# Kernel tuning notes

Measured on AMD Instinct MI355X. Metric: run time of the kernel, lower is better.

Reference implementation:

```python
import jax, jax.numpy as jnp
import numpy as np

VTH = 1.0      # v_threshold
TAU = 2.0      # spikingjelly LIFNode default tau
ALPHA = 2.0    # ATan surrogate alpha
EPS = 1e-5     # BatchNorm eps
N_HEADS = 8
TOPK = 4       # routed regions per query region
REGION = 64    # tokens per region (4096 tokens -> 64 regions)


@jax.custom_vjp
def spike_fn(v):
    return (v >= VTH).astype(v.dtype)

def _spike_fwd(v):
    return (v >= VTH).astype(v.dtype), v

def _spike_bwd(v, g):
    sg = (ALPHA / 2.0) / (1.0 + (jnp.pi / 2.0 * ALPHA * (v - VTH)) ** 2)
    return (g * sg,)

spike_fn.defvjp(_spike_fwd, _spike_bwd)


def lif(x):
    # x: [T, B, L, D]; LIF with decay_input=True, hard reset to 0, detach_reset
    def step(v, xt):
        v = v + (xt - v) / TAU
        s = spike_fn(v)
        v = v * (1.0 - jax.lax.stop_gradient(s))
        return v, s
    _, s = jax.lax.scan(step, jnp.zeros_like(x[0]), x)
    return s


def batchnorm(x, gamma, beta):
    # torch BN1d over [T*B, D, L] in training mode == per-channel stats over (T,B,L)
    mean = x.mean(axis=(0, 1, 2))
    var = jnp.mean((x - mean) ** 2, axis=(0, 1, 2))
    return (x - mean) * jax.lax.rsqrt(var + EPS) * gamma + beta


def bilevel_attn(x, qkv_w, qkv_b, proj_w, proj_b):
    # x: [TB, L, D]
    TB, L, D = x.shape
    nreg = L // REGION
    hd = D // N_HEADS
    qkv = x @ qkv_w.T + qkv_b
    q, k, v = jnp.split(qkv, 3, axis=-1)
    qr = q.reshape(TB, nreg, REGION, D)
    kr = k.reshape(TB, nreg, REGION, D)
    vr = v.reshape(TB, nreg, REGION, D)
    # coarse region-level routing via mean-pooled q/k affinity
    aff = jnp.einsum('bnd,bmd->bnm', qr.mean(2), kr.mean(2))  # [TB, nreg, nreg]
    _, idx = jax.lax.top_k(aff, TOPK)                         # [TB, nreg, TOPK]
    gather = jax.vmap(lambda t, ix: t[ix])                    # per-sample region gather
    kg = gather(kr, idx).reshape(TB, nreg, TOPK * REGION, N_HEADS, hd)
    vg = gather(vr, idx).reshape(TB, nreg, TOPK * REGION, N_HEADS, hd)
    qh = qr.reshape(TB, nreg, REGION, N_HEADS, hd)
    logits = jnp.einsum('bnqhd,bnkhd->bnhqk', qh, kg) * (hd ** -0.5)
    p = jax.nn.softmax(logits, axis=-1)
    o = jnp.einsum('bnhqk,bnkhd->bnqhd', p, vg).reshape(TB, L, D)
    return o @ proj_w.T + proj_b


def setup_inputs() -> dict:
    key = jax.random.key(0)
    ks = jax.random.split(key, 8)
    T, B, Lt, L, D = 4, 2, 4, 1024, 256
    Ltot = Lt * L
    s = 0.02
    return {
        'x': jax.random.normal(ks[0], (T, B, Ltot, D), jnp.float32),
        'bn1_g': jnp.ones((D,), jnp.float32),
        'bn1_b': jnp.zeros((D,), jnp.float32),
        'bn2_g': jnp.ones((D,), jnp.float32),
        'bn2_b': jnp.zeros((D,), jnp.float32),
        'qkv_w': jax.random.normal(ks[1], (3 * D, D), jnp.float32) * s,
        'qkv_b': jnp.zeros((3 * D,), jnp.float32),
        'proj_w': jax.random.normal(ks[2], (D, D), jnp.float32) * s,
        'proj_b': jnp.zeros((D,), jnp.float32),
        'ffn_w1': jax.random.normal(ks[3], (4 * D, D), jnp.float32) * s,
        'ffn_b1': jnp.zeros((4 * D,), jnp.float32),
        'ffn_w2': jax.random.normal(ks[4], (D, 4 * D), jnp.float32) * s,
        'ffn_b2': jnp.zeros((D,), jnp.float32),
        'scale': jnp.ones((1,), jnp.float32) * 0.5,
        'Lt': Lt, 'b': B, 'L': L, 'dim': D,
    }


def reference(x, bn1_g, bn1_b, bn2_g, bn2_b, qkv_w, qkv_b, proj_w, proj_b,
              ffn_w1, ffn_b1, ffn_w2, ffn_b2, scale, Lt, b, L, dim):
    T = x.shape[0]
    Ltot = Lt * L
    # attention branch
    identity = x
    s1 = lif(batchnorm(x, bn1_g, bn1_b))
    a = bilevel_attn(s1.reshape(T * b, Ltot, dim), qkv_w, qkv_b, proj_w, proj_b)
    x = identity + a.reshape(T, b, Ltot, dim) * scale
    # ffn branch
    s2 = lif(batchnorm(x, bn2_g, bn2_b))
    h = jax.nn.gelu(s2 @ ffn_w1.T + ffn_b1, approximate=False) @ ffn_w2.T + ffn_b2
    return x + h * scale
```

## Files before the change

kernel.cpp:

```cpp
#include <hip/hip_runtime.h>
#include <hip/hip_bf16.h>
#include <math.h>

typedef __attribute__((ext_vector_type(8))) short short8;
typedef __attribute__((ext_vector_type(4))) float f32x4;

#define DIM 256
#define NROWS 32768
#define PERT 2097152
#define SAMP_TOK 4096

__device__ __forceinline__ float b2f(__hip_bfloat16 h){ return __bfloat162float(h); }
__device__ __forceinline__ __hip_bfloat16 f2b(float f){ return __float2bfloat16(f); }
__device__ __forceinline__ unsigned short f2bu(float f){
  __hip_bfloat16 h = __float2bfloat16(f);
  unsigned short u; __builtin_memcpy(&u, &h, 2); return u;
}

#define GLD_LDS16(gp, lp) __builtin_amdgcn_global_load_lds( \
    (const __attribute__((address_space(1))) unsigned int*)(gp), \
    (__attribute__((address_space(3))) unsigned int*)(lp), 16, 0, 0)

__device__ __forceinline__ float gelu_fast(float v){
  float z  = v * 0.70710678118654752f;
  float az = fabsf(z);
  float t  = __builtin_amdgcn_rcpf(fmaf(0.3275911f, az, 1.0f));
  float p  = fmaf(fmaf(fmaf(fmaf(1.061405429f, t, -1.453152027f), t,
                            1.421413741f), t, -0.284496736f), t, 0.254829592f);
  p *= t;
  float e  = __expf(-z * z);
  float y  = fmaf(-p, e, 1.0f);
  return fmaf(0.5f * fabsf(v), y, 0.5f * v);
}

__global__ void f2b_k(const float* __restrict__ in, __hip_bfloat16* __restrict__ out, int n){
  int i = blockIdx.x * 256 + threadIdx.x;
  if (i < n) out[i] = f2b(in[i]);
}

__global__ void bn_stats_k(const float* __restrict__ x, float* __restrict__ sum, float* __restrict__ sumsq){
  int c = threadIdx.x;
  size_t base = (size_t)blockIdx.x * 64 * DIM + c;
  float s = 0.f, s2 = 0.f;
  for (int i = 0; i < 64; ++i){
    float v = x[base + (size_t)i * DIM];
    s += v; s2 += v * v;
  }
  atomicAdd(&sum[c], s);
  atomicAdd(&sumsq[c], s2);
}

__global__ void bn_fin_k(const float* __restrict__ sum, const float* __restrict__ sumsq,
                         const float* __restrict__ g, const float* __restrict__ b,
                         float* __restrict__ a_out, float* __restrict__ b_out){
  int c = threadIdx.x;
  float mean = sum[c] * (1.f/32768.f);
  float var  = sumsq[c] * (1.f/32768.f) - mean*mean;
  float a = g[c] / sqrtf(var + 1e-5f);
  a_out[c] = a;
  b_out[c] = b[c] - mean * a;
}

__global__ void lif_k(const float* __restrict__ x, const float* __restrict__ av,
                      const float* __restrict__ bv, __hip_bfloat16* __restrict__ s){
  int e = blockIdx.x * blockDim.x + threadIdx.x;
  if (e >= PERT) return;
  int c = e & (DIM - 1);
  float a = av[c], b = bv[c];
  float v = 0.f;
  #pragma unroll
  for (int t = 0; t < 4; ++t){
    float xn = x[(size_t)t * PERT + e] * a + b;
    v += (xn - v) * 0.5f;
    float sp = (v >= 1.0f) ? 1.0f : 0.0f;
    s[(size_t)t * PERT + e] = f2b(sp);
    v = (v >= 1.0f) ? 0.f : v;
  }
}

__global__ void region_sum_k(const __hip_bfloat16* __restrict__ s, float* __restrict__ sm){
  int r = blockIdx.x, c = threadIdx.x;
  float acc = 0.f;
  size_t base = (size_t)r * 64 * DIM + c;
  for (int i = 0; i < 64; ++i) acc += b2f(s[base + (size_t)i * DIM]);
  sm[(size_t)r * DIM + c] = acc * 0.015625f;
}

__global__ void rgemm_k(const float* __restrict__ smr, const float* __restrict__ w,
                        const float* __restrict__ bias, float* __restrict__ qkm){
  __shared__ float arow[256];
  int r = blockIdx.x, t = threadIdx.x;
  arow[t] = smr[(size_t)r * 256 + t];
  __syncthreads();
  for (int j = t; j < 512; j += 256){
    const float* wr = w + (size_t)j * 256;
    float acc = 0.f;
    for (int k = 0; k < 256; ++k) acc += arow[k] * wr[k];
    qkm[(size_t)r * 512 + j] = acc + bias[j];
  }
}

template<int EPI>
__global__ __launch_bounds__(256) void gemm_bt(
    const __hip_bfloat16* __restrict__ A, const __hip_bfloat16* __restrict__ W,
    const float* __restrict__ bias, void* __restrict__ outp,
    const void* __restrict__ extra, const float* __restrict__ scaleptr,
    int K, int N)
{
  __shared__ __align__(16) short As[128 * 32];
  __shared__ __align__(16) short Ws[128 * 32];
  int tid = threadIdx.x;
  int bm = blockIdx.x, bn = blockIdx.y;
  int lane = tid & 63;
  int l16 = lane & 15, quad = lane >> 4;
  int wv = tid >> 6;
  int wm = (wv >> 1) << 6, wn = (wv & 1) << 6;

  const __hip_bfloat16* Ag = A + (size_t)(bm * 128 + (tid >> 2)) * K + ((tid & 3) << 3);
  const __hip_bfloat16* Wg = W + (size_t)(bn * 128 + (tid >> 2)) * K + ((tid & 3) << 3);
  short* Ad = As + tid * 8;
  short* Wd = Ws + tid * 8;
  const size_t rstep = (size_t)64 * K;

  f32x4 zero = {0.f, 0.f, 0.f, 0.f};
  f32x4 acc[4][4];
  #pragma unroll
  for (int i = 0; i < 4; ++i)
    #pragma unroll
    for (int j = 0; j < 4; ++j) acc[i][j] = zero;

  for (int k0 = 0; k0 < K; k0 += 32){
    GLD_LDS16(Ag + k0,         Ad);
    GLD_LDS16(Ag + rstep + k0, Ad + 2048);
    GLD_LDS16(Wg + k0,         Wd);
    GLD_LDS16(Wg + rstep + k0, Wd + 2048);
    __syncthreads();
    short8 af[4];
    #pragma unroll
    for (int mi = 0; mi < 4; ++mi)
      af[mi] = *reinterpret_cast<const short8*>(&As[(wm + mi * 16 + l16) * 32 + (quad << 3)]);
    #pragma unroll
    for (int ni = 0; ni < 4; ++ni){
      short8 wf = *reinterpret_cast<const short8*>(&Ws[(wn + ni * 16 + l16) * 32 + (quad << 3)]);
      #pragma unroll
      for (int mi = 0; mi < 4; ++mi)
        acc[mi][ni] = __builtin_amdgcn_mfma_f32_16x16x32_bf16(wf, af[mi], acc[mi][ni], 0, 0, 0);
    }
    __syncthreads();
  }

  float sc = 0.f;
  if (EPI == 1 || EPI == 3) sc = scaleptr[0];
  #pragma unroll
  for (int ni = 0; ni < 4; ++ni){
    int col0 = (bn << 7) + wn + ni * 16 + (quad << 2);
    float4 bv = *reinterpret_cast<const float4*>(bias + col0);
    #pragma unroll
    for (int mi = 0; mi < 4; ++mi){
      int rowg = (bm << 7) + wm + mi * 16 + l16;
      size_t off = (size_t)rowg * N + col0;
      float v0 = acc[mi][ni][0] + bv.x;
      float v1 = acc[mi][ni][1] + bv.y;
      float v2 = acc[mi][ni][2] + bv.z;
      float v3 = acc[mi][ni][3] + bv.w;
      if (EPI == 0){
        unsigned lo = (unsigned)f2bu(v0) | ((unsigned)f2bu(v1) << 16);
        unsigned hi = (unsigned)f2bu(v2) | ((unsigned)f2bu(v3) << 16);
        *reinterpret_cast<uint2*>((__hip_bfloat16*)outp + off) = make_uint2(lo, hi);
      } else if (EPI == 1 || EPI == 3){
        float4 xr = *reinterpret_cast<const float4*>((const float*)extra + off);
        float4 ov;
        ov.x = xr.x + v0 * sc; ov.y = xr.y + v1 * sc;
        ov.z = xr.z + v2 * sc; ov.w = xr.w + v3 * sc;
        *reinterpret_cast<float4*>((float*)outp + off) = ov;
      } else {
        float g0 = gelu_fast(v0), g1 = gelu_fast(v1);
        float g2 = gelu_fast(v2), g3 = gelu_fast(v3);
        unsigned lo = (unsigned)f2bu(g0) | ((unsigned)f2bu(g1) << 16);
        unsigned hi = (unsigned)f2bu(g2) | ((unsigned)f2bu(g3) << 16);
        *reinterpret_cast<uint2*>((__hip_bfloat16*)outp + off) = make_uint2(lo, hi);
      }
    }
  }
}

__global__ void topk_k(const float* __restrict__ qkm, int* __restrict__ idx){
  __shared__ float aff[64];
  int r = blockIdx.x;
  int m = threadIdx.x;
  int b = r >> 6;
  const float4* qrow = reinterpret_cast<const float4*>(qkm + (size_t)r * 512);
  const float4* krow = reinterpret_cast<const float4*>(qkm + (size_t)(b * 64 + m) * 512 + 256);
  float dot = 0.f;
  for (int d = 0; d < 64; ++d){
    float4 qv = qrow[d], kv = krow[d];
    dot += qv.x * kv.x + qv.y * kv.y + qv.z * kv.z + qv.w * kv.w;
  }
  aff[m] = dot;
  __syncthreads();
  if (m == 0){
    #pragma unroll
    for (int t = 0; t < 4; ++t){
      float best = -INFINITY; int bi = 0;
      for (int i = 0; i < 64; ++i){
        if (aff[i] > best){ best = aff[i]; bi = i; }
      }
      aff[bi] = -INFINITY;
      idx[r * 4 + t] = bi;
    }
  }
}

__global__ __launch_bounds__(256) void attn_mfma_k(
    const __hip_bfloat16* __restrict__ qkv, const int* __restrict__ idx,
    __hip_bfloat16* __restrict__ o_out, int rbase)
{
  __shared__ __align__(16) short lds[27136];
  __shared__ float den_s[4][16];
  const int rl = blockIdx.x;
  const int h  = blockIdx.y;
  const int rg = rbase + rl;
  const int bl = rl >> 6;
  const int tid = threadIdx.x;
  const int w = tid >> 6, lane = tid & 63;
  const int l16 = lane & 15, quad = lane >> 4;
  short* Pw = lds + 10240 + w * 4224;

  const int reg = idx[rg * 4 + (tid >> 6)] & 63;
  const size_t srow = (size_t)bl * SAMP_TOK + (size_t)reg * 64 + (tid & 63);
  const __hip_bfloat16* kvsrc = qkv + srow * 768 + 256 + (size_t)h * 32;

  const size_t qrow = (size_t)rl * 64 + w * 16 + l16;
  short8 qf = *reinterpret_cast<const short8*>(qkv + qrow * 768 + (size_t)h * 32 + quad * 8);

  uint4 vreg[4];
  #pragma unroll
  for (int c = 0; c < 4; ++c)
    vreg[c] = *reinterpret_cast<const uint4*>(kvsrc + 256 + c * 8);

  #pragma unroll
  for (int c = 0; c < 4; ++c)
    *reinterpret_cast<uint4*>(&lds[tid * 40 + c * 8]) =
      *reinterpret_cast<const uint4*>(kvsrc + c * 8);
  __syncthreads();

  f32x4 s[16];
  #pragma unroll
  for (int nt = 0; nt < 16; ++nt){
    short8 bf = *reinterpret_cast<const short8*>(&lds[(nt * 16 + l16) * 40 + quad * 8]);
    f32x4 z = {0.f, 0.f, 0.f, 0.f};
    s[nt] = __builtin_amdgcn_mfma_f32_16x16x32_bf16(qf, bf, z, 0, 0, 0);
  }
  __syncthreads();

  #pragma unroll
  for (int c = 0; c < 4; ++c){
    short8 vv = *reinterpret_cast<short8*>(&vreg[c]);
    #pragma unroll
    for (int e = 0; e < 8; ++e)
      lds[(c * 8 + e) * 264 + tid] = vv[e];
  }

  float m4[4] = {-1e30f, -1e30f, -1e30f, -1e30f};
  #pragma unroll
  for (int nt = 0; nt < 16; ++nt)
    #pragma unroll
    for (int r = 0; r < 4; ++r) m4[r] = fmaxf(m4[r], s[nt][r]);
  #pragma unroll
  for (int xm = 1; xm < 16; xm <<= 1)
    #pragma unroll
    for (int r = 0; r < 4; ++r) m4[r] = fmaxf(m4[r], __shfl_xor(m4[r], xm));
  float d4[4] = {0.f, 0.f, 0.f, 0.f};
  #pragma unroll
  for (int nt = 0; nt < 16; ++nt)
    #pragma unroll
    for (int r = 0; r < 4; ++r){
      float e = __expf((s[nt][r] - m4[r]) * 0.17677669529663687f);
      s[nt][r] = e; d4[r] += e;
    }
  #pragma unroll
  for (int xm = 1; xm < 16; xm <<= 1)
    #pragma unroll
    for (int r = 0; r < 4; ++r) d4[r] += __shfl_xor(d4[r], xm);
  if (l16 == 0){
    #pragma unroll
    for (int r = 0; r < 4; ++r) den_s[w][quad * 4 + r] = d4[r];
  }
  #pragma unroll
  for (int nt = 0; nt < 16; ++nt)
    #pragma unroll
    for (int r = 0; r < 4; ++r)
      Pw[(quad * 4 + r) * 264 + nt * 16 + l16] = (short)f2bu(s[nt][r]);
  __syncthreads();

  f32x4 o0 = {0.f, 0.f, 0.f, 0.f}, o1 = o0;
  #pragma unroll
  for (int kk = 0; kk < 8; ++kk){
    short8 pb = *reinterpret_cast<const short8*>(&Pw[l16 * 264 + kk * 32 + quad * 8]);
    short8 a0 = *reinterpret_cast<const short8*>(&lds[l16 * 264 + kk * 32 + quad * 8]);
    short8 a1 = *reinterpret_cast<const short8*>(&lds[(16 + l16) * 264 + kk * 32 + quad * 8]);
    o0 = __builtin_amdgcn_mfma_f32_16x16x32_bf16(a0, pb, o0, 0, 0, 0);
    o1 = __builtin_amdgcn_mfma_f32_16x16x32_bf16(a1, pb, o1, 0, 0, 0);
  }
  float inv = 1.f / den_s[w][l16];
  size_t obase = ((size_t)rl * 64 + w * 16 + l16) * 256 + (size_t)h * 32;
  unsigned pk0 = (unsigned)f2bu(o0[0] * inv) | ((unsigned)f2bu(o0[1] * inv) << 16);
  unsigned pk1 = (unsigned)f2bu(o0[2] * inv) | ((unsigned)f2bu(o0[3] * inv) << 16);
  unsigned pk2 = (unsigned)f2bu(o1[0] * inv) | ((unsigned)f2bu(o1[1] * inv) << 16);
  unsigned pk3 = (unsigned)f2bu(o1[2] * inv) | ((unsigned)f2bu(o1[3] * inv) << 16);
  *reinterpret_cast<uint2*>(o_out + obase + quad * 4)      = make_uint2(pk0, pk1);
  *reinterpret_cast<uint2*>(o_out + obase + 16 + quad * 4) = make_uint2(pk2, pk3);
}

extern "C" void kernel_launch(void* const* d_in, const int* in_sizes, int n_in,
                              void* d_out, int out_size, void* d_ws, size_t ws_size,
                              hipStream_t stream)
{
  const float* x      = (const float*)d_in[0];
  const float* bn1_g  = (const float*)d_in[1];
  const float* bn1_b  = (const float*)d_in[2];
  const float* bn2_g  = (const float*)d_in[3];
  const float* bn2_b  = (const float*)d_in[4];
  const float* qkv_w  = (const float*)d_in[5];
  const float* qkv_b  = (const float*)d_in[6];
  const float* proj_w = (const float*)d_in[7];
  const float* proj_b = (const float*)d_in[8];
  const float* ffn_w1 = (const float*)d_in[9];
  const float* ffn_b1 = (const float*)d_in[10];
  const float* ffn_w2 = (const float*)d_in[11];
  const float* ffn_b2 = (const float*)d_in[12];
  const float* scale  = (const float*)d_in[13];
  float* x2 = (float*)d_out;

  char* ws = (char*)d_ws;
  const size_t MB = 1024 * 1024;
  float* sum1 = (float*)(ws + 0);
  float* sq1  = (float*)(ws + 1024);
  float* sum2 = (float*)(ws + 2048);
  float* sq2  = (float*)(ws + 3072);
  float* a1   = (float*)(ws + 4096);
  float* b1   = (float*)(ws + 5120);
  float* a2   = (float*)(ws + 6144);
  float* b2   = (float*)(ws + 7168);
  int*   idxb = (int*)(ws + 8192);
  float* smr  = (float*)(ws + 16384);
  float* qkm  = (float*)(ws + 540672);
  __hip_bfloat16* qkv_wb  = (__hip_bfloat16*)(ws + 1589248);
  __hip_bfloat16* proj_wb = (__hip_bfloat16*)(ws + 1982464);
  __hip_bfloat16* ffn_w1b = (__hip_bfloat16*)(ws + 2113536);
  __hip_bfloat16* ffn_w2b = (__hip_bfloat16*)(ws + 2637824);
  __hip_bfloat16* s1 = (__hip_bfloat16*)(ws + 4 * MB);
  __hip_bfloat16* s2 = s1;
  char* chunkbuf = ws + 20 * MB;

  size_t avail = (ws_size > 20 * MB) ? (ws_size - 20 * MB) : (8 * MB);
  int nc = (avail >= 64 * MB) ? 8 : (avail >= 32 * MB) ? 4 : (avail >= 16 * MB) ? 2 : 1;
  int crows = 32768;
  while ((size_t)crows * 2048 > avail && crows > 2048) crows >>= 1;

  __hip_bfloat16* qkvc = (__hip_bfloat16*)chunkbuf;
  __hip_bfloat16* oc   = (__hip_bfloat16*)(chunkbuf + (size_t)nc * 6 * MB);
  __hip_bfloat16* h1   = (__hip_bfloat16*)chunkbuf;

  hipMemsetAsync(d_ws, 0, 4096, stream);

  f2b_k<<<(196608 + 255) / 256, 256, 0, stream>>>(qkv_w, qkv_wb, 196608);
  f2b_k<<<(65536 + 255) / 256, 256, 0, stream>>>(proj_w, proj_wb, 65536);
  f2b_k<<<(262144 + 255) / 256, 256, 0, stream>>>(ffn_w1, ffn_w1b, 262144);
  f2b_k<<<(262144 + 255) / 256, 256, 0, stream>>>(ffn_w2, ffn_w2b, 262144);

  bn_stats_k<<<512, 256, 0, stream>>>(x, sum1, sq1);
  bn_fin_k<<<1, 256, 0, stream>>>(sum1, sq1, bn1_g, bn1_b, a1, b1);
  lif_k<<<PERT / 256, 256, 0, stream>>>(x, a1, b1, s1);
  region_sum_k<<<512, 256, 0, stream>>>(s1, smr);
  rgemm_k<<<512, 256, 0, stream>>>(smr, qkv_w, qkv_b, qkm);
  topk_k<<<512, 64, 0, stream>>>(qkm, idxb);

  const int nchunkA = 8 / nc;
  for (int c = 0; c < nchunkA; ++c){
    const size_t ro = (size_t)c * nc * SAMP_TOK;
    gemm_bt<0><<<dim3(nc * SAMP_TOK / 128, 6), 256, 0, stream>>>(
        s1 + ro * 256, qkv_wb, qkv_b, qkvc, nullptr, nullptr, 256, 768);
    attn_mfma_k<<<dim3(nc * 64, 8), 256, 0, stream>>>(qkvc, idxb, oc, c * nc * 64);
    gemm_bt<1><<<dim3(nc * SAMP_TOK / 128, 2), 256, 0, stream>>>(
        oc, proj_wb, proj_b, x2 + ro * 256, x + ro * 256, scale, 256, 256);
  }

  bn_stats_k<<<512, 256, 0, stream>>>(x2, sum2, sq2);
  bn_fin_k<<<1, 256, 0, stream>>>(sum2, sq2, bn2_g, bn2_b, a2, b2);
  lif_k<<<PERT / 256, 256, 0, stream>>>(x2, a2, b2, s2);
  const int nchunkF = 32768 / crows;
  for (int c = 0; c < nchunkF; ++c){
    const size_t ro = (size_t)c * crows;
    gemm_bt<2><<<dim3(crows / 128, 8), 256, 0, stream>>>(
        s2 + ro * 256, ffn_w1b, ffn_b1, h1, nullptr, nullptr, 256, 1024);
    gemm_bt<3><<<dim3(crows / 128, 2), 256, 0, stream>>>(
        h1, ffn_w2b, ffn_b2, x2 + ro * 256, x2 + ro * 256, scale, 1024, 256);
  }
}
```

Measured before the change: 399.1 us.

## Double-buffer GEMM LDS tiles with XOR swizzle and fuse weight casts

The bf16 GEMM kernel now uses two LDS buffers, so the global-to-LDS load of the next K slice is issued while MFMAs run on the current one. An XOR swizzle on the 16-byte column chunk, applied on both the load and read side, is meant to reduce LDS bank conflicts. The four weight fp32->bf16 conversion launches are merged into one kernel to cut launch overhead. LDS use per block doubles, which may lower occupancy.

```diff
diff --git a/kernel.cpp b/kernel.cpp
--- a/kernel.cpp
+++ b/kernel.cpp
@@ -33,9 +33,15 @@
   return fmaf(0.5f * fabsf(v), y, 0.5f * v);
 }
 
-__global__ void f2b_k(const float* __restrict__ in, __hip_bfloat16* __restrict__ out, int n){
+__global__ void f2ball_k(const float* __restrict__ w_qkv, const float* __restrict__ w_proj,
+                         const float* __restrict__ w_f1, const float* __restrict__ w_f2,
+                         __hip_bfloat16* __restrict__ o_qkv, __hip_bfloat16* __restrict__ o_proj,
+                         __hip_bfloat16* __restrict__ o_f1, __hip_bfloat16* __restrict__ o_f2){
   int i = blockIdx.x * 256 + threadIdx.x;
-  if (i < n) out[i] = f2b(in[i]);
+  if (i < 196608)          o_qkv[i]           = f2b(w_qkv[i]);
+  else if (i < 262144)     o_proj[i - 196608] = f2b(w_proj[i - 196608]);
+  else if (i < 524288)     o_f1[i - 262144]   = f2b(w_f1[i - 262144]);
+  else                     o_f2[i - 524288]   = f2b(w_f2[i - 524288]);
 }
 
 __global__ void bn_stats_k(const float* __restrict__ x, float* __restrict__ sum, float* __restrict__ sumsq){
@@ -107,8 +113,10 @@
     const void* __restrict__ extra, const float* __restrict__ scaleptr,
     int K, int N)
 {
-  __shared__ __align__(16) short As[128 * 32];
-  __shared__ __align__(16) short Ws[128 * 32];
+  __shared__ __align__(16) short As0[128 * 32];
+  __shared__ __align__(16) short Ws0[128 * 32];
+  __shared__ __align__(16) short As1[128 * 32];
+  __shared__ __align__(16) short Ws1[128 * 32];
   int tid = threadIdx.x;
   int bm = blockIdx.x, bn = blockIdx.y;
   int lane = tid & 63;
@@ -116,11 +124,20 @@
   int wv = tid >> 6;
   int wm = (wv >> 1) << 6, wn = (wv & 1) << 6;
 
-  const __hip_bfloat16* Ag = A + (size_t)(bm * 128 + (tid >> 2)) * K + ((tid & 3) << 3);
-  const __hip_bfloat16* Wg = W + (size_t)(bn * 128 + (tid >> 2)) * K + ((tid & 3) << 3);
-  short* Ad = As + tid * 8;
-  short* Wd = Ws + tid * 8;
+  const int srow = tid >> 2;
+  const int sq   = (tid & 3) ^ ((srow >> 1) & 3);
+  const __hip_bfloat16* Ag = A + (size_t)(bm * 128 + srow) * K + (sq << 3);
+  const __hip_bfloat16* Wg = W + (size_t)(bn * 128 + srow) * K + (sq << 3);
   const size_t rstep = (size_t)64 * K;
+
+  int roA[4], roW[4];
+  #pragma unroll
+  for (int i = 0; i < 4; ++i){
+    int Ra = wm + i * 16 + l16;
+    roA[i] = Ra * 32 + ((quad ^ ((Ra >> 1) & 3)) << 3);
+    int Rw = wn + i * 16 + l16;
+    roW[i] = Rw * 32 + ((quad ^ ((Rw >> 1) & 3)) << 3);
+  }
 
   f32x4 zero = {0.f, 0.f, 0.f, 0.f};
   f32x4 acc[4][4];
@@ -129,23 +146,34 @@
     #pragma unroll
     for (int j = 0; j < 4; ++j) acc[i][j] = zero;
 
-  for (int k0 = 0; k0 < K; k0 += 32){
-    GLD_LDS16(Ag + k0,         Ad);
-    GLD_LDS16(Ag + rstep + k0, Ad + 2048);
-    GLD_LDS16(Wg + k0,         Wd);
-    GLD_LDS16(Wg + rstep + k0, Wd + 2048);
-    __syncthreads();
+  auto stage = [&](short* Ad, short* Wd, int k0){
+    GLD_LDS16(Ag + k0,         Ad + tid * 8);
+    GLD_LDS16(Ag + rstep + k0, Ad + tid * 8 + 2048);
+    GLD_LDS16(Wg + k0,         Wd + tid * 8);
+    GLD_LDS16(Wg + rstep + k0, Wd + tid * 8 + 2048);
+  };
+  auto compute = [&](const short* Asb, const short* Wsb){
     short8 af[4];
     #pragma unroll
     for (int mi = 0; mi < 4; ++mi)
-      af[mi] = *reinterpret_cast<const short8*>(&As[(wm + mi * 16 + l16) * 32 + (quad << 3)]);
+      af[mi] = *reinterpret_cast<const short8*>(Asb + roA[mi]);
     #pragma unroll
     for (int ni = 0; ni < 4; ++ni){
-      short8 wf = *reinterpret_cast<const short8*>(&Ws[(wn + ni * 16 + l16) * 32 + (quad << 3)]);
+      short8 wf = *reinterpret_cast<const short8*>(Wsb + roW[ni]);
       #pragma unroll
       for (int mi = 0; mi < 4; ++mi)
         acc[mi][ni] = __builtin_amdgcn_mfma_f32_16x16x32_bf16(wf, af[mi], acc[mi][ni], 0, 0, 0);
     }
+  };
+
+  stage(As0, Ws0, 0);
+  __syncthreads();
+  for (int k0 = 0; k0 < K; k0 += 64){
+    if (k0 + 32 < K) stage(As1, Ws1, k0 + 32);
+    compute(As0, Ws0);
+    __syncthreads();
+    if (k0 + 64 < K) stage(As0, Ws0, k0 + 64);
+    if (k0 + 32 < K) compute(As1, Ws1);
     __syncthreads();
   }
 
@@ -364,10 +392,8 @@
 
   hipMemsetAsync(d_ws, 0, 4096, stream);
 
-  f2b_k<<<(196608 + 255) / 256, 256, 0, stream>>>(qkv_w, qkv_wb, 196608);
-  f2b_k<<<(65536 + 255) / 256, 256, 0, stream>>>(proj_w, proj_wb, 65536);
-  f2b_k<<<(262144 + 255) / 256, 256, 0, stream>>>(ffn_w1, ffn_w1b, 262144);
-  f2b_k<<<(262144 + 255) / 256, 256, 0, stream>>>(ffn_w2, ffn_w2b, 262144);
+  f2ball_k<<<3072, 256, 0, stream>>>(qkv_w, proj_w, ffn_w1, ffn_w2,
+                                     qkv_wb, proj_wb, ffn_w1b, ffn_w2b);
 
   bn_stats_k<<<512, 256, 0, stream>>>(x, sum1, sq1);
   bn_fin_k<<<1, 256, 0, stream>>>(sum1, sq1, bn1_g, bn1_b, a1, b1);
```

Result: faster. 386.1 us (-3.3%).
